# Kernel tuning notes

Hardware: AMD Instinct MI355X
Metric: run time of the kernel (lower is better)

## Reference

```python
import jax, jax.numpy as jnp
import numpy as np

NUM_HEADS = 16
EPS = 1e-5


def _ln(x, w, b):
    mu = jnp.mean(x, axis=-1, keepdims=True)
    var = jnp.mean((x - mu) ** 2, axis=-1, keepdims=True)
    return (x - mu) * jax.lax.rsqrt(var + EPS) * w + b


def _ada_ln(x, vol, lw, lb, gamma, beta, vs_w, vs_b):
    y = _ln(x, lw, lb)
    # volatility_scale: Linear(1,1) on vol[..., None] -> sigmoid
    vs = jax.nn.sigmoid(vol[..., None] * vs_w + vs_b)  # (B,S,1)
    return y * (1.0 + vs) * gamma + beta


def setup_inputs() -> dict:
    key = jax.random.key(0)
    ks = jax.random.split(key, 20)
    B, S, H = 8, 1024, 1024
    Hf = 4 * H
    Hg = H // 2
    w = lambda k, i, o: jax.random.normal(k, (i, o), jnp.float32) * 0.02
    inp = {
        'x': jax.random.normal(ks[0], (B, S, H), jnp.float32),
        'volatility': jax.random.uniform(ks[1], (B, S), jnp.float32),
        'Wq': w(ks[2], H, H), 'bq': jnp.zeros((H,), jnp.float32),
        'Wk': w(ks[3], H, H), 'bk': jnp.zeros((H,), jnp.float32),
        'Wv': w(ks[4], H, H), 'bv': jnp.zeros((H,), jnp.float32),
        'Wo': w(ks[5], H, H), 'bo': jnp.zeros((H,), jnp.float32),
        'ln1_w': jnp.ones((H,), jnp.float32), 'ln1_b': jnp.zeros((H,), jnp.float32),
        'gamma1': jnp.ones((), jnp.float32), 'beta1': jnp.zeros((), jnp.float32),
        'vs1_w': jnp.float32(0.3), 'vs1_b': jnp.float32(0.0),
        'ffn_w1': w(ks[6], H, Hf), 'ffn_b1': jnp.zeros((Hf,), jnp.float32),
        'ffn_w2': w(ks[7], Hf, H), 'ffn_b2': jnp.zeros((H,), jnp.float32),
        'gate_w1': w(ks[8], H, Hg), 'gate_b1': jnp.zeros((Hg,), jnp.float32),
        'gate_w2': w(ks[9], Hg, H), 'gate_b2': jnp.zeros((H,), jnp.float32),
        'ln2_w': jnp.ones((H,), jnp.float32), 'ln2_b': jnp.zeros((H,), jnp.float32),
        'gamma2': jnp.ones((), jnp.float32), 'beta2': jnp.zeros((), jnp.float32),
        'vs2_w': jnp.float32(0.3), 'vs2_b': jnp.float32(0.0),
    }
    return inp


def reference(x, volatility, Wq, bq, Wk, bk, Wv, bv, Wo, bo,
              ln1_w, ln1_b, gamma1, beta1, vs1_w, vs1_b,
              ffn_w1, ffn_b1, ffn_w2, ffn_b2,
              gate_w1, gate_b1, gate_w2, gate_b2,
              ln2_w, ln2_b, gamma2, beta2, vs2_w, vs2_b):
    B, S, H = x.shape
    nh = NUM_HEADS
    hd = H // nh
    scale = np.sqrt(hd).astype(np.float32)

    # self-attention (eval mode -> dropout is identity)
    Q = (x @ Wq + bq).reshape(B, S, nh, hd)
    K = (x @ Wk + bk).reshape(B, S, nh, hd)
    V = (x @ Wv + bv).reshape(B, S, nh, hd)
    scores = jnp.einsum('bqhd,bkhd->bhqk', Q, K) / scale
    attn = jax.nn.softmax(scores, axis=-1)
    ctx = jnp.einsum('bhqk,bkhd->bqhd', attn, V).reshape(B, S, H)
    attn_out = ctx @ Wo + bo

    x = x + attn_out
    x = _ada_ln(x, volatility, ln1_w, ln1_b, gamma1, beta1, vs1_w, vs1_b)

    # volatility-adaptive FFN (volatility present -> gated path)
    h = jax.nn.gelu(x @ ffn_w1 + ffn_b1, approximate=False)
    ffn_out = h @ ffn_w2 + ffn_b2
    g = jax.nn.sigmoid(jax.nn.relu(x @ gate_w1 + gate_b1) @ gate_w2 + gate_b2)
    ffn_res = ffn_out * g + x * (1.0 - g)

    x = x + ffn_res
    x = _ada_ln(x, volatility, ln2_w, ln2_b, gamma2, beta2, vs2_w, vs2_b)
    return x
```

## Files before the change

kernel.cpp:

```cpp
#include <hip/hip_runtime.h>
#include <hip/hip_bf16.h>
#include <math.h>


#define HDIM 1024
#define NHEAD 16
#define DHEAD 64
#define NBATCH 8
#define NSEQ 1024
#define NTOK (NBATCH * NSEQ)
#define QKVSTR 3072
#define LNEPS 1e-5f
#define LOG2E_8 0.180336880f

using f32x4 = __attribute__((ext_vector_type(4))) float;
using s16x8 = __attribute__((ext_vector_type(8))) short;
using u16x8 = __attribute__((ext_vector_type(8))) unsigned short;

enum { ACT_NONE = 0, ACT_GELU = 1, ACT_RELU = 2, ACT_SIG = 3 };

__device__ inline float bf2f(unsigned short u) {
    union { unsigned u; float f; } t; t.u = ((unsigned)u) << 16; return t.f;
}
__device__ inline unsigned short f2bf(float f) {
    __hip_bfloat16 h = __float2bfloat16(f);
    return *reinterpret_cast<unsigned short*>(&h);
}
__device__ inline float gelu_f(float t) {
    const float u = t * (0.7978845608f + 0.0356774081f * t * t);
    const float e = __expf(2.f * u);
    const float th = 1.f - 2.f / (e + 1.f);
    return 0.5f * t * (1.f + th);
}

#define GLDS16(g, l) __builtin_amdgcn_global_load_lds( \
    (__attribute__((address_space(1))) void*)(g),      \
    (__attribute__((address_space(3))) void*)(l), 16, 0, 0)

__global__ __launch_bounds__(256)
void cast_bf16_k(const float* __restrict__ in, unsigned short* __restrict__ out, int n4)
{
    for (int i = blockIdx.x * 256 + threadIdx.x; i < n4; i += gridDim.x * 256) {
        float4 v = ((const float4*)in)[i];
        ushort4 o;
        o.x = f2bf(v.x); o.y = f2bf(v.y); o.z = f2bf(v.z); o.w = f2bf(v.w);
        ((ushort4*)out)[i] = o;
    }
}

__global__ __launch_bounds__(256)
void concat3_k(const float* __restrict__ a, const float* __restrict__ b,
               const float* __restrict__ c, float* __restrict__ o)
{
    int i = blockIdx.x * 256 + threadIdx.x;
    o[i] = i < 1024 ? a[i] : (i < 2048 ? b[i - 1024] : c[i - 2048]);
}

__global__ __launch_bounds__(256)
void transpose_cast_k(const float* __restrict__ W, unsigned short* __restrict__ Wt,
                      int K, int N)
{
    __shared__ float tile[32][33];
    const int tx = threadIdx.x, ty = threadIdx.y;
    const int k0 = blockIdx.y * 32, n0 = blockIdx.x * 32;
#pragma unroll
    for (int r = 0; r < 32; r += 8)
        tile[ty + r][tx] = W[(size_t)(k0 + ty + r) * N + n0 + tx];
    __syncthreads();
#pragma unroll
    for (int r = 0; r < 32; r += 8)
        Wt[(size_t)(n0 + ty + r) * K + k0 + tx] = f2bf(tile[tx][ty + r]);
}

__global__ __launch_bounds__(256)
void transpose_cast4_k(const float* __restrict__ W0, const float* __restrict__ W1,
                       const float* __restrict__ W2, const float* __restrict__ W3,
                       unsigned short* __restrict__ Wt)
{
    __shared__ float tile[32][33];
    const int z = blockIdx.z;
    const float* W = z == 0 ? W0 : z == 1 ? W1 : z == 2 ? W2 : W3;
    unsigned short* dst = Wt + (size_t)z * HDIM * HDIM;
    const int tx = threadIdx.x, ty = threadIdx.y;
    const int k0 = blockIdx.y * 32, n0 = blockIdx.x * 32;
#pragma unroll
    for (int r = 0; r < 32; r += 8)
        tile[ty + r][tx] = W[(size_t)(k0 + ty + r) * HDIM + n0 + tx];
    __syncthreads();
#pragma unroll
    for (int r = 0; r < 32; r += 8)
        dst[(size_t)(n0 + ty + r) * HDIM + k0 + tx] = f2bf(tile[tx][ty + r]);
}

__global__ __launch_bounds__(256)
void transpose_v_k(const unsigned short* __restrict__ vb, unsigned short* __restrict__ vtb)
{
    __shared__ unsigned short t[64][72];
    const int tid = threadIdx.x;
    const int b = blockIdx.z, h = blockIdx.y;
    const int s0 = blockIdx.x * 64;
    {
        const int r = tid >> 3, c = (tid & 7) * 8;
        *(u16x8*)&t[r][c] =
            *(const u16x8*)&vb[((size_t)(b * NSEQ + s0 + r)) * QKVSTR + h * DHEAD + c];
        *(u16x8*)&t[r + 32][c] =
            *(const u16x8*)&vb[((size_t)(b * NSEQ + s0 + r + 32)) * QKVSTR + h * DHEAD + c];
    }
    __syncthreads();
    {
        const int d = tid & 63, sc = (tid >> 6) * 16;
        u16x8 o0, o1;
#pragma unroll
        for (int i = 0; i < 8; ++i) o0[i] = t[sc + i][d];
#pragma unroll
        for (int i = 0; i < 8; ++i) o1[i] = t[sc + 8 + i][d];
        unsigned short* dst = &vtb[((size_t)((b * NHEAD + h) * DHEAD + d)) * NSEQ + s0 + sc];
        *(u16x8*)dst = o0;
        *(u16x8*)(dst + 8) = o1;
    }
}

template<int BM, int BN, int ACT, bool HAS_ADD, bool OUT_BF>
__global__ __launch_bounds__(512, (BM == 128) ? 4 : 2)
void gemm8_k(const unsigned short* __restrict__ A, const unsigned short* __restrict__ Bt,
             const float* __restrict__ bias, const float* __restrict__ add,
             void* __restrict__ Cv, int M, int N, int K)
{
    extern __shared__ __align__(16) unsigned short lds[];
    constexpr int BK = 64;
    constexpr int WN = (BN == 256) ? 4 : 2;
    constexpr int WM = 8 / WN;
    constexpr int MREP = BM / (WM * 16);
    constexpr int NREP = BN / (WN * 16);
    constexpr int ASZ = BM * BK;
    constexpr int BSZ = BN * BK;
    constexpr int AR = BM / 64;
    constexpr int BR = BN / 64;
    constexpr int VM = AR + BR;
    constexpr int NPH = (BN == 256) ? 4 : 2;
    constexpr int MI_PER = MREP / 2;
    constexpr int NJ_PER = (BN == 256) ? 2 : 4;

    const int tid = threadIdx.x;
    const int lane = tid & 63;
    const int w = tid >> 6;
    const int wr = w / WN;
    const int wc = w % WN;
    const int m0 = blockIdx.y * BM;
    const int n0 = blockIdx.x * BN;
    const int fr = lane & 15;
    const int fo = lane >> 4;

    const int srow = tid >> 3;
    const int sslot = (tid & 7) ^ (srow & 7);
    const size_t a_base = (size_t)(m0 + srow) * K + sslot * 8;
    const size_t b_base = (size_t)(n0 + srow) * K + sslot * 8;

    f32x4 acc[MREP][NREP] = {};

    auto stage = [&](int t) {
        const int buf = t & 1;
        unsigned short* ad = lds + buf * ASZ + w * 512;
        unsigned short* bd = lds + 2 * ASZ + buf * BSZ + w * 512;
        const unsigned short* as_ = A + a_base + (size_t)t * BK;
        const unsigned short* bs_ = Bt + b_base + (size_t)t * BK;
#pragma unroll
        for (int j = 0; j < AR; ++j)
            GLDS16(as_ + (size_t)j * 64 * K, ad + j * 4096);
#pragma unroll
        for (int j = 0; j < BR; ++j)
            GLDS16(bs_ + (size_t)j * 64 * K, bd + j * 4096);
    };

    const int NT = K / BK;
    stage(0);

    for (int t = 0; t < NT; ++t) {
        if (t + 1 < NT) {
            stage(t + 1);
            asm volatile("s_waitcnt vmcnt(%0)" :: "i"(VM) : "memory");
        } else {
            asm volatile("s_waitcnt vmcnt(0)" ::: "memory");
        }
        __builtin_amdgcn_s_barrier();

        const char* Ab = (const char*)(lds + (t & 1) * ASZ);
        const char* Bb = (const char*)(lds + 2 * ASZ + (t & 1) * BSZ);

        s16x8 af[MI_PER][2], bfr[NJ_PER][2];
#pragma unroll
        for (int ph = 0; ph < NPH; ++ph) {
            const int mh = (BN == 256) ? ((ph == 1 || ph == 2) ? 1 : 0) : ph;
            const int nh = (BN == 256) ? (ph >> 1) : 0;
            const bool la = (BN != 256) || (ph != 2);
            const bool lb = (BN == 256) ? ((ph & 1) == 0) : (ph == 0);
            if (la) {
#pragma unroll
                for (int i = 0; i < MI_PER; ++i) {
                    const int row = wr * (BM / WM) + (mh * MI_PER + i) * 16 + fr;
                    const int sw = (row & 7) << 4;
#pragma unroll
                    for (int kk = 0; kk < 2; ++kk)
                        af[i][kk] = *(const s16x8*)(Ab + row * 128 + ((kk * 64 + fo * 16) ^ sw));
                }
            }
            if (lb) {
#pragma unroll
                for (int j = 0; j < NJ_PER; ++j) {
                    const int row = wc * 64 + (nh * NJ_PER + j) * 16 + fr;
                    const int sw = (row & 7) << 4;
#pragma unroll
                    for (int kk = 0; kk < 2; ++kk)
                        bfr[j][kk] = *(const s16x8*)(Bb + row * 128 + ((kk * 64 + fo * 16) ^ sw));
                }
            }
            __builtin_amdgcn_s_setprio(1);
#pragma unroll
            for (int i = 0; i < MI_PER; ++i)
#pragma unroll
                for (int j = 0; j < NJ_PER; ++j)
#pragma unroll
                    for (int kk = 0; kk < 2; ++kk)
                        acc[mh * MI_PER + i][nh * NJ_PER + j] =
                            __builtin_amdgcn_mfma_f32_16x16x32_bf16(
                                af[i][kk], bfr[j][kk],
                                acc[mh * MI_PER + i][nh * NJ_PER + j], 0, 0, 0);
            __builtin_amdgcn_s_setprio(0);
        }
        asm volatile("s_waitcnt lgkmcnt(0)" ::: "memory");
        __builtin_amdgcn_sched_barrier(0);
        __builtin_amdgcn_s_barrier();
    }

    float bv[NREP];
#pragma unroll
    for (int j = 0; j < NREP; ++j)
        bv[j] = bias[n0 + wc * 64 + j * 16 + fr];
#pragma unroll
    for (int i = 0; i < MREP; ++i) {
#pragma unroll
        for (int j = 0; j < NREP; ++j) {
            const int gn = n0 + wc * 64 + j * 16 + fr;
#pragma unroll
            for (int r = 0; r < 4; ++r) {
                const int gm = m0 + wr * (BM / WM) + i * 16 + fo * 4 + r;
                float t = acc[i][j][r] + bv[j];
                if (HAS_ADD) t += add[(size_t)gm * N + gn];
                if (ACT == ACT_GELU)      t = gelu_f(t);
                else if (ACT == ACT_RELU) t = fmaxf(t, 0.f);
                else if (ACT == ACT_SIG)  t = 1.f / (1.f + __expf(-t));
                if (OUT_BF) ((unsigned short*)Cv)[(size_t)gm * N + gn] = f2bf(t);
                else        ((float*)Cv)[(size_t)gm * N + gn] = t;
            }
        }
    }
}

__global__ __launch_bounds__(256)
void attn_k(const unsigned short* __restrict__ QKVb, const unsigned short* __restrict__ Vtb,
            unsigned short* __restrict__ Cb)
{
    __shared__ alignas(16) unsigned short Ks[2][64 * 64];
    __shared__ alignas(16) unsigned short Vs[2][64 * 64];
    __shared__ alignas(16) unsigned short Ps[4][16 * 72];

    const int tid = threadIdx.x;
    const int lane = tid & 63;
    const int wid = tid >> 6;
    const int L = blockIdx.x;
    const int xcd = L & 7, slot = L >> 3;
    const int bh = xcd + ((slot >> 4) << 3);
    const int qt = slot & 15;
    const int b = bh >> 4, h = bh & 15;
    const int q0 = qt * 64 + wid * 16;

    const int kcol = lane & 15;
    const int kofs = (lane >> 4) * 8;
    const size_t qoff = ((size_t)(b * NSEQ + q0 + kcol)) * QKVSTR + h * DHEAD + kofs;
    const s16x8 qf0 = *(const s16x8*)(QKVb + qoff);
    const s16x8 qf1 = *(const s16x8*)(QKVb + qoff + 32);

    f32x4 accO[4] = {};
    float mrow[4] = {-1e30f, -1e30f, -1e30f, -1e30f};
    float lrow[4] = {0.f, 0.f, 0.f, 0.f};

    const int lr = lane >> 3;
    const int swz8 = (((lane & 7) ^ lr)) * 8;
    const size_t kbase  = ((size_t)(b * NSEQ)) * QKVSTR + HDIM + h * DHEAD;
    const size_t vtbase = ((size_t)(bh * DHEAD)) * NSEQ;

    unsigned short* const pw = &Ps[wid][0];
    const int prow = (lane >> 4) * 4;

    auto stage = [&](int kt, int buf) {
#pragma unroll
        for (int j = 0; j < 2; ++j) {
            const int rowb = wid * 16 + j * 8;
            GLDS16(QKVb + kbase + (size_t)(kt * 64 + rowb + lr) * QKVSTR + swz8,
                   Ks[buf] + rowb * 64);
            GLDS16(Vtb + vtbase + (size_t)(rowb + lr) * NSEQ + kt * 64 + swz8,
                   Vs[buf] + rowb * 64);
        }
    };

    stage(0, 0);
    asm volatile("s_waitcnt vmcnt(0)" ::: "memory");
    __syncthreads();

    for (int kt = 0; kt < NSEQ / 64; ++kt) {
        const int cur = kt & 1;
        if (kt + 1 < NSEQ / 64) stage(kt + 1, cur ^ 1);

        f32x4 sa[4];
#pragma unroll
        for (int jt = 0; jt < 4; ++jt) {
            const int kr = jt * 16 + kcol;
            const unsigned swz = ((unsigned)(kr & 7)) << 4;
            const s16x8 kf0 = *(const s16x8*)((const char*)Ks[cur] + kr * 128 + ((kofs * 2) ^ swz));
            const s16x8 kf1 = *(const s16x8*)((const char*)Ks[cur] + kr * 128 + ((64 + kofs * 2) ^ swz));
            f32x4 t = {};
            t = __builtin_amdgcn_mfma_f32_16x16x32_bf16(qf0, kf0, t, 0, 0, 0);
            t = __builtin_amdgcn_mfma_f32_16x16x32_bf16(qf1, kf1, t, 0, 0, 0);
            sa[jt] = t * LOG2E_8;
        }

        float mx[4];
#pragma unroll
        for (int r = 0; r < 4; ++r) {
            float m = fmaxf(fmaxf(sa[0][r], sa[1][r]), fmaxf(sa[2][r], sa[3][r]));
            m = fmaxf(m, __shfl_xor(m, 1));
            m = fmaxf(m, __shfl_xor(m, 2));
            m = fmaxf(m, __shfl_xor(m, 4));
            m = fmaxf(m, __shfl_xor(m, 8));
            mx[r] = m;
        }
        float dmax = fmaxf(fmaxf(mx[0] - mrow[0], mx[1] - mrow[1]),
                           fmaxf(mx[2] - mrow[2], mx[3] - mrow[3]));
        if (!__all(dmax <= 8.f)) {
#pragma unroll
            for (int r = 0; r < 4; ++r) {
                const float mn = fmaxf(mrow[r], mx[r]);
                const float corr = exp2f(mrow[r] - mn);
                mrow[r] = mn;
                lrow[r] *= corr;
#pragma unroll
                for (int dt = 0; dt < 4; ++dt) accO[dt][r] *= corr;
            }
        }
#pragma unroll
        for (int r = 0; r < 4; ++r) {
            float ps = 0.f;
#pragma unroll
            for (int jt = 0; jt < 4; ++jt) {
                const float p = exp2f(sa[jt][r] - mrow[r]);
                pw[(prow + r) * 72 + jt * 16 + kcol] = f2bf(p);
                ps += p;
            }
            ps += __shfl_xor(ps, 1);
            ps += __shfl_xor(ps, 2);
            ps += __shfl_xor(ps, 4);
            ps += __shfl_xor(ps, 8);
            lrow[r] += ps;
        }

#pragma unroll
        for (int kc = 0; kc < 2; ++kc) {
            const s16x8 pa = *(const s16x8*)(pw + kcol * 72 + kc * 32 + kofs);
#pragma unroll
            for (int dt = 0; dt < 4; ++dt) {
                const int dr = dt * 16 + kcol;
                const unsigned swz = ((unsigned)(dr & 7)) << 4;
                const s16x8 vf = *(const s16x8*)((const char*)Vs[cur] + dr * 128 +
                                                 ((kc * 64 + kofs * 2) ^ swz));
                accO[dt] = __builtin_amdgcn_mfma_f32_16x16x32_bf16(pa, vf, accO[dt], 0, 0, 0);
            }
        }

        if (kt + 1 < NSEQ / 64) asm volatile("s_waitcnt vmcnt(0)" ::: "memory");
        __builtin_amdgcn_s_barrier();
    }

    const size_t obase = ((size_t)(b * NSEQ + q0 + prow)) * HDIM + h * DHEAD;
#pragma unroll
    for (int r = 0; r < 4; ++r) {
        const float rl = 1.f / lrow[r];
#pragma unroll
        for (int dt = 0; dt < 4; ++dt)
            Cb[obase + (size_t)r * HDIM + dt * 16 + kcol] = f2bf(accO[dt][r] * rl);
    }
}

template<int MODE, bool WRITE_BF>
__global__ __launch_bounds__(256)
void adaln_k(const float* __restrict__ a, const float* __restrict__ fo,
             const float* __restrict__ g, const float* __restrict__ vol,
             const float* __restrict__ lw, const float* __restrict__ lb,
             const float* __restrict__ gm, const float* __restrict__ bt,
             const float* __restrict__ vsw, const float* __restrict__ vsb,
             float* __restrict__ out, unsigned short* __restrict__ out_bf)
{
    const int tok = blockIdx.x;
    const int tid = threadIdx.x;
    const size_t base = (size_t)tok * HDIM + tid * 4;
    float v[4];
    {
        float4 va = *(const float4*)&a[base];
        if (MODE == 1) {
            float4 vf = *(const float4*)&fo[base];
            float4 vg = *(const float4*)&g[base];
            v[0] = va.x * (2.f - vg.x) + vf.x * vg.x;
            v[1] = va.y * (2.f - vg.y) + vf.y * vg.y;
            v[2] = va.z * (2.f - vg.z) + vf.z * vg.z;
            v[3] = va.w * (2.f - vg.w) + vf.w * vg.w;
        } else {
            v[0] = va.x; v[1] = va.y; v[2] = va.z; v[3] = va.w;
        }
    }
    float sum = v[0] + v[1] + v[2] + v[3];
    float sq  = v[0]*v[0] + v[1]*v[1] + v[2]*v[2] + v[3]*v[3];
#pragma unroll
    for (int off = 32; off > 0; off >>= 1) {
        sum += __shfl_down(sum, off);
        sq  += __shfl_down(sq, off);
    }
    __shared__ float ssum[4], ssq[4];
    const int wid = tid >> 6, lane = tid & 63;
    if (lane == 0) { ssum[wid] = sum; ssq[wid] = sq; }
    __syncthreads();
    const float tsum = ssum[0] + ssum[1] + ssum[2] + ssum[3];
    const float tsq  = ssq[0]  + ssq[1]  + ssq[2]  + ssq[3];
    const float mu   = tsum * (1.f / 1024.f);
    const float var  = tsq * (1.f / 1024.f) - mu * mu;
    const float rstd = rsqrtf(var + LNEPS);
    const float vsv  = 1.f / (1.f + __expf(-(vol[tok] * vsw[0] + vsb[0])));
    const float sca  = (1.f + vsv) * gm[0];
    const float off2 = bt[0];
    const float4 lwv = *(const float4*)&lw[tid * 4];
    const float4 lbv = *(const float4*)&lb[tid * 4];
    float r0 = ((v[0] - mu) * rstd * lwv.x + lbv.x) * sca + off2;
    float r1 = ((v[1] - mu) * rstd * lwv.y + lbv.y) * sca + off2;
    float r2 = ((v[2] - mu) * rstd * lwv.z + lbv.z) * sca + off2;
    float r3 = ((v[3] - mu) * rstd * lwv.w + lbv.w) * sca + off2;
    *(float4*)&out[base] = make_float4(r0, r1, r2, r3);
    if (WRITE_BF) {
        ushort4 ob;
        ob.x = f2bf(r0); ob.y = f2bf(r1); ob.z = f2bf(r2); ob.w = f2bf(r3);
        *(ushort4*)&out_bf[base] = ob;
    }
}

extern "C" void kernel_launch(void* const* d_in, const int* in_sizes, int n_in,
                              void* d_out, int out_size, void* d_ws, size_t ws_size,
                              hipStream_t stream)
{
    (void)in_sizes; (void)n_in; (void)out_size; (void)ws_size;
    const float* x    = (const float*)d_in[0];
    const float* vol  = (const float*)d_in[1];
    const float* Wq   = (const float*)d_in[2];  const float* bq  = (const float*)d_in[3];
    const float* Wk   = (const float*)d_in[4];  const float* bk  = (const float*)d_in[5];
    const float* Wv   = (const float*)d_in[6];  const float* bv  = (const float*)d_in[7];
    const float* Wo   = (const float*)d_in[8];  const float* bo  = (const float*)d_in[9];
    const float* ln1w = (const float*)d_in[10]; const float* ln1b = (const float*)d_in[11];
    const float* gm1  = (const float*)d_in[12]; const float* be1 = (const float*)d_in[13];
    const float* vs1w = (const float*)d_in[14]; const float* vs1b = (const float*)d_in[15];
    const float* fw1  = (const float*)d_in[16]; const float* fb1 = (const float*)d_in[17];
    const float* fw2  = (const float*)d_in[18]; const float* fb2 = (const float*)d_in[19];
    const float* gw1  = (const float*)d_in[20]; const float* gb1 = (const float*)d_in[21];
    const float* gw2  = (const float*)d_in[22]; const float* gb2 = (const float*)d_in[23];
    const float* ln2w = (const float*)d_in[24]; const float* ln2b = (const float*)d_in[25];
    const float* gm2  = (const float*)d_in[26]; const float* be2 = (const float*)d_in[27];
    const float* vs2w = (const float*)d_in[28]; const float* vs2b = (const float*)d_in[29];

    char* w = (char*)d_ws;
    auto MB = [](size_t v) { return v << 20; };
    unsigned short* wtqkv = (unsigned short*)(w + MB(0));
    unsigned short* wto   = (unsigned short*)(w + MB(6));
    unsigned short* wtf1  = (unsigned short*)(w + MB(8));
    unsigned short* wtf2  = (unsigned short*)(w + MB(16));
    unsigned short* wtg1  = (unsigned short*)(w + MB(24));
    unsigned short* wtg2  = (unsigned short*)(w + MB(25));
    unsigned short* xb   = (unsigned short*)(w + MB(26));
    unsigned short* qkvb = (unsigned short*)(w + MB(42));
    unsigned short* vtb  = (unsigned short*)(w + MB(90));
    unsigned short* cxb  = (unsigned short*)(w + MB(106));
    float*          ao   = (float*)(w + MB(122));
    float*          x1   = (float*)(w + MB(42));
    unsigned short* x1b  = (unsigned short*)(w + MB(74));
    unsigned short* hb   = (unsigned short*)(w + MB(90));
    float*          ffn  = (float*)(w + MB(154));
    unsigned short* ghb  = (unsigned short*)(w + MB(26));
    float*          gg   = (float*)(w + MB(90));
    float*          bqkv = (float*)(w + MB(186));

    dim3 blk(256);
    dim3 tb(32, 8);
    transpose_cast4_k<<<dim3(32, 32, 4), tb, 0, stream>>>(Wq, Wk, Wv, Wo, wtqkv);
    transpose_cast_k<<<dim3(4096/32, 1024/32), tb, 0, stream>>>(fw1, wtf1, 1024, 4096);
    transpose_cast_k<<<dim3(1024/32, 4096/32), tb, 0, stream>>>(fw2, wtf2, 4096, 1024);
    transpose_cast_k<<<dim3(512/32, 1024/32),  tb, 0, stream>>>(gw1, wtg1, 1024, 512);
    transpose_cast_k<<<dim3(1024/32, 512/32),  tb, 0, stream>>>(gw2, wtg2, 512, 1024);
    cast_bf16_k<<<2048, blk, 0, stream>>>(x, xb, NTOK * HDIM / 4);
    concat3_k<<<12, blk, 0, stream>>>(bq, bk, bv, bqkv);

    const size_t SH128 = (128 + 128) * 256;
    const size_t SH256 = (256 + 256) * 256;
    gemm8_k<128, 128, ACT_NONE, false, true><<<dim3(24, 64), 512, SH128, stream>>>(
        xb, wtqkv, bqkv, nullptr, qkvb, NTOK, QKVSTR, HDIM);
    transpose_v_k<<<dim3(NSEQ / 64, NHEAD, NBATCH), blk, 0, stream>>>(qkvb + 2048, vtb);
    attn_k<<<dim3(2048), blk, 0, stream>>>(qkvb, vtb, cxb);
    gemm8_k<128, 128, ACT_NONE, true, false><<<dim3(8, 64), 512, SH128, stream>>>(
        cxb, wto, bo, x, ao, NTOK, HDIM, HDIM);
    adaln_k<0, true><<<dim3(NTOK), blk, 0, stream>>>(
        ao, nullptr, nullptr, vol, ln1w, ln1b, gm1, be1, vs1w, vs1b, x1, x1b);
    gemm8_k<256, 256, ACT_GELU, false, true><<<dim3(16, 32), 512, SH256, stream>>>(
        x1b, wtf1, fb1, nullptr, hb, NTOK, 4096, HDIM);
    gemm8_k<128, 128, ACT_NONE, false, false><<<dim3(8, 64), 512, SH128, stream>>>(
        hb, wtf2, fb2, nullptr, ffn, NTOK, HDIM, 4096);
    gemm8_k<128, 128, ACT_RELU, false, true><<<dim3(4, 64), 512, SH128, stream>>>(
        x1b, wtg1, gb1, nullptr, ghb, NTOK, 512, HDIM);
    gemm8_k<128, 128, ACT_SIG, false, false><<<dim3(8, 64), 512, SH128, stream>>>(
        ghb, wtg2, gb2, nullptr, gg, NTOK, HDIM, 512);
    adaln_k<1, false><<<dim3(NTOK), blk, 0, stream>>>(
        x1, ffn, gg, vol, ln2w, ln2b, gm2, be2, vs2w, vs2b, (float*)d_out, nullptr);
}
```

Before: 504.0 us.

## Widen attention blocks to 8 waves and defer softmax row reductions

```diff
diff --git a/kernel.cpp b/kernel.cpp
--- a/kernel.cpp
+++ b/kernel.cpp
@@ -256,23 +256,23 @@
     }
 }
 
-__global__ __launch_bounds__(256)
+__global__ __launch_bounds__(512, 6)
 void attn_k(const unsigned short* __restrict__ QKVb, const unsigned short* __restrict__ Vtb,
             unsigned short* __restrict__ Cb)
 {
     __shared__ alignas(16) unsigned short Ks[2][64 * 64];
     __shared__ alignas(16) unsigned short Vs[2][64 * 64];
-    __shared__ alignas(16) unsigned short Ps[4][16 * 72];
+    __shared__ alignas(16) unsigned short Ps[8][16 * 72];
 
     const int tid = threadIdx.x;
     const int lane = tid & 63;
     const int wid = tid >> 6;
     const int L = blockIdx.x;
-    const int xcd = L & 7, slot = L >> 3;
-    const int bh = xcd + ((slot >> 4) << 3);
-    const int qt = slot & 15;
+    const int xcd = L & 7, s = L >> 3;
+    const int bh = xcd + ((s >> 3) << 3);
+    const int qt = s & 7;
     const int b = bh >> 4, h = bh & 15;
-    const int q0 = qt * 64 + wid * 16;
+    const int q0 = qt * 128 + wid * 16;
 
     const int kcol = lane & 15;
     const int kofs = (lane >> 4) * 8;
@@ -282,7 +282,7 @@
 
     f32x4 accO[4] = {};
     float mrow[4] = {-1e30f, -1e30f, -1e30f, -1e30f};
-    float lrow[4] = {0.f, 0.f, 0.f, 0.f};
+    float lsum[4] = {0.f, 0.f, 0.f, 0.f};
 
     const int lr = lane >> 3;
     const int swz8 = (((lane & 7) ^ lr)) * 8;
@@ -293,14 +293,11 @@
     const int prow = (lane >> 4) * 4;
 
     auto stage = [&](int kt, int buf) {
-#pragma unroll
-        for (int j = 0; j < 2; ++j) {
-            const int rowb = wid * 16 + j * 8;
-            GLDS16(QKVb + kbase + (size_t)(kt * 64 + rowb + lr) * QKVSTR + swz8,
-                   Ks[buf] + rowb * 64);
-            GLDS16(Vtb + vtbase + (size_t)(rowb + lr) * NSEQ + kt * 64 + swz8,
-                   Vs[buf] + rowb * 64);
-        }
+        const int rowb = wid * 8;
+        GLDS16(QKVb + kbase + (size_t)(kt * 64 + rowb + lr) * QKVSTR + swz8,
+               Ks[buf] + rowb * 64);
+        GLDS16(Vtb + vtbase + (size_t)(rowb + lr) * NSEQ + kt * 64 + swz8,
+               Vs[buf] + rowb * 64);
     };
 
     stage(0, 0);
@@ -324,43 +321,36 @@
             sa[jt] = t * LOG2E_8;
         }
 
-        float mx[4];
-#pragma unroll
-        for (int r = 0; r < 4; ++r) {
-            float m = fmaxf(fmaxf(sa[0][r], sa[1][r]), fmaxf(sa[2][r], sa[3][r]));
-            m = fmaxf(m, __shfl_xor(m, 1));
-            m = fmaxf(m, __shfl_xor(m, 2));
-            m = fmaxf(m, __shfl_xor(m, 4));
-            m = fmaxf(m, __shfl_xor(m, 8));
-            mx[r] = m;
-        }
-        float dmax = fmaxf(fmaxf(mx[0] - mrow[0], mx[1] - mrow[1]),
-                           fmaxf(mx[2] - mrow[2], mx[3] - mrow[3]));
-        if (!__all(dmax <= 8.f)) {
+        float lmax[4];
+#pragma unroll
+        for (int r = 0; r < 4; ++r)
+            lmax[r] = fmaxf(fmaxf(sa[0][r], sa[1][r]), fmaxf(sa[2][r], sa[3][r]));
+        const float guard = fmaxf(fmaxf(lmax[0] - mrow[0], lmax[1] - mrow[1]),
+                                  fmaxf(lmax[2] - mrow[2], lmax[3] - mrow[3]));
+        if (!__all(guard <= 8.f)) {
 #pragma unroll
             for (int r = 0; r < 4; ++r) {
-                const float mn = fmaxf(mrow[r], mx[r]);
+                float m = lmax[r];
+                m = fmaxf(m, __shfl_xor(m, 1));
+                m = fmaxf(m, __shfl_xor(m, 2));
+                m = fmaxf(m, __shfl_xor(m, 4));
+                m = fmaxf(m, __shfl_xor(m, 8));
+                const float mn = fmaxf(mrow[r], m);
                 const float corr = exp2f(mrow[r] - mn);
                 mrow[r] = mn;
-                lrow[r] *= corr;
+                lsum[r] *= corr;
 #pragma unroll
                 for (int dt = 0; dt < 4; ++dt) accO[dt][r] *= corr;
             }
         }
 #pragma unroll
         for (int r = 0; r < 4; ++r) {
-            float ps = 0.f;
 #pragma unroll
             for (int jt = 0; jt < 4; ++jt) {
                 const float p = exp2f(sa[jt][r] - mrow[r]);
                 pw[(prow + r) * 72 + jt * 16 + kcol] = f2bf(p);
-                ps += p;
+                lsum[r] += p;
             }
-            ps += __shfl_xor(ps, 1);
-            ps += __shfl_xor(ps, 2);
-            ps += __shfl_xor(ps, 4);
-            ps += __shfl_xor(ps, 8);
-            lrow[r] += ps;
         }
 
 #pragma unroll
@@ -380,10 +370,18 @@
         __builtin_amdgcn_s_barrier();
     }
 
+#pragma unroll
+    for (int r = 0; r < 4; ++r) {
+        lsum[r] += __shfl_xor(lsum[r], 1);
+        lsum[r] += __shfl_xor(lsum[r], 2);
+        lsum[r] += __shfl_xor(lsum[r], 4);
+        lsum[r] += __shfl_xor(lsum[r], 8);
+    }
+
     const size_t obase = ((size_t)(b * NSEQ + q0 + prow)) * HDIM + h * DHEAD;
 #pragma unroll
     for (int r = 0; r < 4; ++r) {
-        const float rl = 1.f / lrow[r];
+        const float rl = 1.f / lsum[r];
 #pragma unroll
         for (int dt = 0; dt < 4; ++dt)
             Cb[obase + (size_t)r * HDIM + dt * 16 + kcol] = f2bf(accO[dt][r] * rl);
@@ -507,7 +505,7 @@
     gemm8_k<128, 128, ACT_NONE, false, true><<<dim3(24, 64), 512, SH128, stream>>>(
         xb, wtqkv, bqkv, nullptr, qkvb, NTOK, QKVSTR, HDIM);
     transpose_v_k<<<dim3(NSEQ / 64, NHEAD, NBATCH), blk, 0, stream>>>(qkvb + 2048, vtb);
-    attn_k<<<dim3(2048), blk, 0, stream>>>(qkvb, vtb, cxb);
+    attn_k<<<dim3(1024), 512, 0, stream>>>(qkvb, vtb, cxb);
     gemm8_k<128, 128, ACT_NONE, true, false><<<dim3(8, 64), 512, SH128, stream>>>(
         cxb, wto, bo, x, ao, NTOK, HDIM, HDIM);
     adaln_k<0, true><<<dim3(NTOK), blk, 0, stream>>>(
```

After: 455.9 us. 9.5% less time.
